# Optimization experiments

Measured on AMD Instinct MI355X. Metric: run time of the kernel, lower is better.

Reference implementation:

```python
import jax, jax.numpy as jnp
import numpy as np

CH = 512      # channels
CI = CH // 4  # in_channel = 128
DILS = (1, 4, 8, 12)
GN_GROUPS = 32


def conv2d(x, w, dil=1, pad=0):
    # x: (N,Cin,H,W), w: (Cout,Cin,kh,kw)
    return jax.lax.conv_general_dilated(
        x, w, window_strides=(1, 1), padding=[(pad, pad), (pad, pad)],
        rhs_dilation=(dil, dil),
        dimension_numbers=('NCHW', 'OIHW', 'NCHW'))


def group_norm(x, gamma, beta, groups=GN_GROUPS, eps=1e-5):
    N, C, H, W = x.shape
    xg = x.reshape(N, groups, C // groups, H, W)
    mu = jnp.mean(xg, axis=(2, 3, 4), keepdims=True)
    var = jnp.var(xg, axis=(2, 3, 4), keepdims=True)
    xn = ((xg - mu) * jax.lax.rsqrt(var + eps)).reshape(N, C, H, W)
    return xn * gamma[None, :, None, None] + beta[None, :, None, None]


def dyn_branch(xd, w_cat, d):
    # dynamic filter: (N, 9, H, W), softmax over the K=9 taps per pixel
    f = jax.nn.softmax(conv2d(xd, w_cat, dil=d, pad=d), axis=1)
    N, C, H, W = xd.shape
    xp = jnp.pad(xd, ((0, 0), (0, 0), (d, d), (d, d)))
    # fused unfold + weighted sum: accumulate 9 shifted views * per-pixel weight
    out = jnp.zeros_like(xd)
    k = 0
    for i in range(3):
        for j in range(3):
            out = out + xp[:, :, i * d:i * d + H, j * d:j * d + W] * f[:, k:k + 1]
            k += 1
    return out


def setup_inputs():
    key = jax.random.key(0)
    ks = jax.random.split(key, 16)
    s = 0.05
    return {
        'x': jax.random.normal(ks[0], (4, CH, 128, 128), jnp.float32),
        'w_scale1': jax.random.normal(ks[1], (CI, CH, 1, 1), jnp.float32) * s,
        'gn1_g': jnp.ones((CI,), jnp.float32),
        'gn1_b': jnp.zeros((CI,), jnp.float32),
        'w_cata': jax.random.normal(ks[2], (9, CI, 3, 3), jnp.float32) * s,
        'w_catb': jax.random.normal(ks[3], (9, CI, 3, 3), jnp.float32) * s,
        'w_catc': jax.random.normal(ks[4], (9, CI, 3, 3), jnp.float32) * s,
        'w_catd': jax.random.normal(ks[5], (9, CI, 3, 3), jnp.float32) * s,
        'w_scale2': jax.random.normal(ks[6], (CI, 5 * CI, 1, 1), jnp.float32) * s,
        'gn2_g': jnp.ones((CI,), jnp.float32),
        'gn2_b': jnp.zeros((CI,), jnp.float32),
        'w_scale3': jax.random.normal(ks[7], (CH, CI, 1, 1), jnp.float32) * s,
        'gn3_g': jnp.ones((CH,), jnp.float32),
        'gn3_b': jnp.zeros((CH,), jnp.float32),
    }


def reference(x, w_scale1, gn1_g, gn1_b, w_cata, w_catb, w_catc, w_catd,
              w_scale2, gn2_g, gn2_b, w_scale3, gn3_g, gn3_b):
    # scale1: 1x1 conv -> GN -> ReLU
    xd = jax.nn.relu(group_norm(conv2d(x, w_scale1), gn1_g, gn1_b))
    # four dilated dynamic-filter branches (unfold + softmax-weighted reduce)
    outs = [dyn_branch(xd, w, d)
            for w, d in zip((w_cata, w_catb, w_catc, w_catd), DILS)]
    cat = jnp.concatenate([xd] + outs, axis=1)  # (N, 5*CI, H, W)
    y = jax.nn.relu(group_norm(conv2d(cat, w_scale2), gn2_g, gn2_b))
    y = jax.nn.relu(group_norm(conv2d(y, w_scale3), gn3_g, gn3_b))
    return y
```

## Files before the change

kernel.cpp:

```cpp
#include <hip/hip_runtime.h>
#include <math.h>

#define HW 16384

typedef float f32x4 __attribute__((ext_vector_type(4)));
typedef __bf16 bf16x8 __attribute__((ext_vector_type(8)));
typedef unsigned short u16x4 __attribute__((ext_vector_type(4)));
typedef unsigned short u16x8 __attribute__((ext_vector_type(8)));

__device__ __forceinline__ unsigned short f2bf(float f) {
  unsigned u = __float_as_uint(f);
  u += 0x7fffu + ((u >> 16) & 1u);
  return (unsigned short)(u >> 16);
}
__device__ __forceinline__ float bf2f(unsigned short s) {
  return __uint_as_float(((unsigned)s) << 16);
}

__global__ void prep_kernel(const float* __restrict__ w1, const float* __restrict__ w2,
                            const float* __restrict__ w3,
                            const float* __restrict__ wa, const float* __restrict__ wb,
                            const float* __restrict__ wc, const float* __restrict__ wd,
                            unsigned short* __restrict__ w1b, unsigned short* __restrict__ w2b,
                            unsigned short* __restrict__ w3b, unsigned short* __restrict__ wr) {
  int idx = blockIdx.x * 256 + threadIdx.x;
  if (idx < 65536) { w1b[idx] = f2bf(w1[idx]); }
  else if (idx < 147456) { int j = idx - 65536; w2b[j] = f2bf(w2[j]); }
  else if (idx < 212992) { int j = idx - 147456; w3b[j] = f2bf(w3[j]); }
  else if (idx < 286720) {
    int j = idx - 212992;
    int br = j / 18432, rem = j % 18432;
    int tap = rem / 2048, rem2 = rem % 2048;
    int kt = rem2 / 128, c = rem2 % 128;
    const float* w = (br == 0) ? wa : (br == 1) ? wb : (br == 2) ? wc : wd;
    float v = (kt < 9) ? w[(kt * 128 + c) * 9 + tap] : 0.f;
    wr[j] = f2bf(v);
  }
}

__device__ __forceinline__ void gn_partial_epilogue(
    f32x4 (&acc)[8], int wv, int lane, int t, int n, int blkx,
    float* __restrict__ part, float (*ps)[32], float (*pss)[32]) {
  float gs[8], gss[8];
#pragma unroll
  for (int cb = 0; cb < 8; ++cb) {
    float s = 0.f, ss = 0.f;
#pragma unroll
    for (int r = 0; r < 4; ++r) { float v = acc[cb][r]; s += v; ss += v * v; }
#pragma unroll
    for (int m = 0; m < 4; ++m) {
      const int msk[4] = {1, 2, 16, 32};
      s += __shfl_xor(s, msk[m]); ss += __shfl_xor(ss, msk[m]);
    }
    gs[cb] = s; gss[cb] = ss;
  }
  if (lane < 16 && (lane & 3) == 0) {
    int q = lane >> 2;
#pragma unroll
    for (int cb = 0; cb < 8; ++cb) { ps[wv][cb * 4 + q] = gs[cb]; pss[wv][cb * 4 + q] = gss[cb]; }
  }
  __syncthreads();
  if (t < 32) {
    float a = ps[0][t] + ps[1][t] + ps[2][t] + ps[3][t];
    float b = pss[0][t] + pss[1][t] + pss[2][t] + pss[3][t];
    float* pp = part + ((size_t)(n * 32 + t) * 256 + blkx) * 2;
    pp[0] = a; pp[1] = b;
  }
}

__global__ __launch_bounds__(256) void conv1f_kernel(
    const float* __restrict__ x, const unsigned short* __restrict__ w1b,
    unsigned short* __restrict__ outb, float* __restrict__ part) {
  __shared__ float xs[2][64][68];
  __shared__ float ps[4][32], pss[4][32];
  int t = threadIdx.x;
  int wv = t >> 6, lane = t & 63, lr = lane & 15, lg = lane >> 4;
  int n = blockIdx.y;
  int p0 = blockIdx.x * 64;
  const float* xn = x + (size_t)n * 512 * HW + p0;
  f32x4 acc[8];
#pragma unroll
  for (int cb = 0; cb < 8; ++cb) acc[cb] = (f32x4){0.f, 0.f, 0.f, 0.f};

  int ci_l = t >> 4, px4 = (t & 15) * 4;
  float4 r[4];

#pragma unroll
  for (int pass = 0; pass < 4; ++pass)
    r[pass] = *(const float4*)(xn + (size_t)(pass * 16 + ci_l) * HW + px4);
#pragma unroll
  for (int pass = 0; pass < 4; ++pass) {
    int cl = pass * 16 + ci_l;
    xs[0][px4 + 0][cl] = r[pass].x; xs[0][px4 + 1][cl] = r[pass].y;
    xs[0][px4 + 2][cl] = r[pass].z; xs[0][px4 + 3][cl] = r[pass].w;
  }

  for (int kt = 0; kt < 8; ++kt) {
    int cur = kt & 1;
    if (kt < 7) {
#pragma unroll
      for (int pass = 0; pass < 4; ++pass)
        r[pass] = *(const float4*)(xn + (size_t)((kt + 1) * 64 + pass * 16 + ci_l) * HW + px4);
    }
    __syncthreads();
#pragma unroll
    for (int ks = 0; ks < 2; ++ks) {
      const float* arow = &xs[cur][wv * 16 + lr][ks * 32 + lg * 8];
      float4 a0 = *(const float4*)arow;
      float4 a1 = *(const float4*)(arow + 4);
      bf16x8 a;
      unsigned short us;
      us = f2bf(a0.x); a[0] = *(__bf16*)&us; us = f2bf(a0.y); a[1] = *(__bf16*)&us;
      us = f2bf(a0.z); a[2] = *(__bf16*)&us; us = f2bf(a0.w); a[3] = *(__bf16*)&us;
      us = f2bf(a1.x); a[4] = *(__bf16*)&us; us = f2bf(a1.y); a[5] = *(__bf16*)&us;
      us = f2bf(a1.z); a[6] = *(__bf16*)&us; us = f2bf(a1.w); a[7] = *(__bf16*)&us;
#pragma unroll
      for (int cb = 0; cb < 8; ++cb) {
        bf16x8 b = *(const bf16x8*)(w1b + (size_t)(cb * 16 + lr) * 512
                                    + kt * 64 + ks * 32 + lg * 8);
        acc[cb] = __builtin_amdgcn_mfma_f32_16x16x32_bf16(a, b, acc[cb], 0, 0, 0);
      }
    }
    if (kt < 7) {
#pragma unroll
      for (int pass = 0; pass < 4; ++pass) {
        int cl = pass * 16 + ci_l;
        xs[cur ^ 1][px4 + 0][cl] = r[pass].x; xs[cur ^ 1][px4 + 1][cl] = r[pass].y;
        xs[cur ^ 1][px4 + 2][cl] = r[pass].z; xs[cur ^ 1][px4 + 3][cl] = r[pass].w;
      }
    }
  }
  unsigned short* on = outb + (size_t)n * HW * 640;
#pragma unroll
  for (int cb = 0; cb < 8; ++cb)
#pragma unroll
    for (int r2 = 0; r2 < 4; ++r2)
      on[(size_t)(p0 + wv * 16 + lg * 4 + r2) * 640 + cb * 16 + lr] = f2bf(acc[cb][r2]);
  __syncthreads();
  gn_partial_epilogue(acc, wv, lane, t, n, blockIdx.x, part, ps, pss);
}

template<int K>
__global__ __launch_bounds__(256) void conv_pm_kernel(
    const unsigned short* __restrict__ act, const unsigned short* __restrict__ w,
    unsigned short* __restrict__ outb, float* __restrict__ part, int ldd) {
  __shared__ float ps[4][32], pss[4][32];
  int t = threadIdx.x;
  int wv = t >> 6, lane = t & 63;
  int lr = lane & 15, lg = lane >> 4;
  int n = blockIdx.y;
  int p0 = blockIdx.x * 64 + wv * 16;
  const unsigned short* an = act + (size_t)n * HW * K;
  f32x4 acc[8];
#pragma unroll
  for (int cb = 0; cb < 8; ++cb) acc[cb] = (f32x4){0.f, 0.f, 0.f, 0.f};
  const unsigned short* ap = an + (size_t)(p0 + lr) * K + lg * 8;
  const unsigned short* bp = w + (size_t)lr * K + lg * 8;
#pragma unroll 2
  for (int ks = 0; ks < K / 32; ++ks) {
    bf16x8 a = *(const bf16x8*)(ap + ks * 32);
#pragma unroll
    for (int cb = 0; cb < 8; ++cb) {
      bf16x8 b = *(const bf16x8*)(bp + (size_t)cb * 16 * K + ks * 32);
      acc[cb] = __builtin_amdgcn_mfma_f32_16x16x32_bf16(a, b, acc[cb], 0, 0, 0);
    }
  }
  unsigned short* on = outb + (size_t)n * HW * ldd;
#pragma unroll
  for (int cb = 0; cb < 8; ++cb)
#pragma unroll
    for (int r = 0; r < 4; ++r)
      on[(size_t)(p0 + lg * 4 + r) * ldd + cb * 16 + lr] = f2bf(acc[cb][r]);
  gn_partial_epilogue(acc, wv, lane, t, n, blockIdx.x, part, ps, pss);
}

__global__ __launch_bounds__(1024) void gnf256_kernel(
    const float* __restrict__ part, float* __restrict__ stats) {
  __shared__ float sh[1024], sh2[1024];
  int t = threadIdx.x;
  int tg = t >> 3, sub = t & 7;
  float s = 0.f, ss = 0.f;
  for (int b = sub * 32; b < sub * 32 + 32; ++b) {
    const float* pp = part + ((size_t)tg * 256 + b) * 2;
    s += pp[0]; ss += pp[1];
  }
  sh[t] = s; sh2[t] = ss;
  __syncthreads();
  if (t < 128) {
    float a = 0.f, b2 = 0.f;
#pragma unroll
    for (int i = 0; i < 8; ++i) { a += sh[t * 8 + i]; b2 += sh2[t * 8 + i]; }
    float inv = 1.f / (4.f * HW);
    float mean = a * inv, var = b2 * inv - mean * mean;
    stats[2 * t] = mean; stats[2 * t + 1] = rsqrtf(var + 1e-5f);
  }
}

__global__ __launch_bounds__(256) void gna_ip_kernel(
    unsigned short* __restrict__ dst, const float* __restrict__ stats,
    const float* __restrict__ gamma, const float* __restrict__ beta, int ldd) {
  int idx = blockIdx.x * 256 + threadIdx.x;
  int g = idx & 31;
  int p = (idx >> 5) & (HW - 1);
  int n = idx >> 19;
  unsigned short* ptr = dst + ((size_t)n * HW + p) * ldd + 4 * g;
  u16x4 v = *(u16x4*)ptr;
  int sg = n * 32 + g;
  float mean = stats[2 * sg], rstd = stats[2 * sg + 1];
  float sc0 = rstd * gamma[4 * g + 0], sc1 = rstd * gamma[4 * g + 1];
  float sc2 = rstd * gamma[4 * g + 2], sc3 = rstd * gamma[4 * g + 3];
  float sh0 = beta[4 * g + 0] - mean * sc0, sh1 = beta[4 * g + 1] - mean * sc1;
  float sh2 = beta[4 * g + 2] - mean * sc2, sh3 = beta[4 * g + 3] - mean * sc3;
  u16x4 o;
  o[0] = f2bf(fmaxf(fmaf(bf2f(v[0]), sc0, sh0), 0.f));
  o[1] = f2bf(fmaxf(fmaf(bf2f(v[1]), sc1, sh1), 0.f));
  o[2] = f2bf(fmaxf(fmaf(bf2f(v[2]), sc2, sh2), 0.f));
  o[3] = f2bf(fmaxf(fmaf(bf2f(v[3]), sc3, sh3), 0.f));
  *(u16x4*)ptr = o;
}

__global__ __launch_bounds__(256) void conv3_kernel(
    const unsigned short* __restrict__ y, const unsigned short* __restrict__ w3,
    unsigned short* __restrict__ outb, float* __restrict__ part) {
  int wv = threadIdx.x >> 6, lane = threadIdx.x & 63;
  int lr = lane & 15, lg = lane >> 4;
  int n = blockIdx.y, zc = blockIdx.z;
  int co0 = zc * 128 + wv * 32;
  int p0 = blockIdx.x * 128;
  const unsigned short* yn = y + (size_t)n * HW * 128;
  f32x4 acc[2][8];
#pragma unroll
  for (int pr = 0; pr < 2; ++pr)
#pragma unroll
    for (int cb = 0; cb < 8; ++cb) acc[pr][cb] = (f32x4){0.f, 0.f, 0.f, 0.f};
#pragma unroll
  for (int ks = 0; ks < 4; ++ks) {
    bf16x8 a0 = *(const bf16x8*)(w3 + (size_t)(co0 + lr) * 128 + ks * 32 + lg * 8);
    bf16x8 a1 = *(const bf16x8*)(w3 + (size_t)(co0 + 16 + lr) * 128 + ks * 32 + lg * 8);
#pragma unroll
    for (int cb = 0; cb < 8; ++cb) {
      bf16x8 b = *(const bf16x8*)(yn + (size_t)(p0 + cb * 16 + lr) * 128 + ks * 32 + lg * 8);
      acc[0][cb] = __builtin_amdgcn_mfma_f32_16x16x32_bf16(a0, b, acc[0][cb], 0, 0, 0);
      acc[1][cb] = __builtin_amdgcn_mfma_f32_16x16x32_bf16(a1, b, acc[1][cb], 0, 0, 0);
    }
  }
  unsigned short* on = outb + (size_t)n * 512 * HW;
  float s[2] = {0.f, 0.f}, ss[2] = {0.f, 0.f};
#pragma unroll
  for (int pr = 0; pr < 2; ++pr)
#pragma unroll
    for (int cb = 0; cb < 8; ++cb)
#pragma unroll
      for (int r = 0; r < 4; ++r) {
        float v = acc[pr][cb][r];
        on[(size_t)(co0 + pr * 16 + lg * 4 + r) * HW + p0 + cb * 16 + lr] = f2bf(v);
        s[pr] += v; ss[pr] += v * v;
      }
#pragma unroll
  for (int pr = 0; pr < 2; ++pr) {
    float a = s[pr], b = ss[pr];
    for (int m = 1; m < 64; m <<= 1) { a += __shfl_xor(a, m); b += __shfl_xor(b, m); }
    if (lane == 0) {
      float* pp = part + ((((size_t)n * 4 + zc) * 128 + blockIdx.x) * 8 + wv * 2 + pr) * 2;
      pp[0] = a; pp[1] = b;
    }
  }
}

__global__ __launch_bounds__(1024) void gnf3_kernel(
    const float* __restrict__ part, float* __restrict__ stats) {
  __shared__ float sh[1024], sh2[1024];
  int t = threadIdx.x;
  int e = t >> 3, xbs = t & 7;
  int n = e >> 5, g = e & 31;
  int zc = g >> 3, sub = g & 7;
  float s = 0.f, ss = 0.f;
  for (int xb = xbs * 16; xb < xbs * 16 + 16; ++xb) {
    const float* pp = part + ((((size_t)n * 4 + zc) * 128 + xb) * 8 + sub) * 2;
    s += pp[0]; ss += pp[1];
  }
  sh[t] = s; sh2[t] = ss;
  __syncthreads();
  if (t < 128) {
    float a = 0.f, b2 = 0.f;
#pragma unroll
    for (int i = 0; i < 8; ++i) { a += sh[t * 8 + i]; b2 += sh2[t * 8 + i]; }
    float inv = 1.f / (16.f * HW);
    float mean = a * inv, var = b2 * inv - mean * mean;
    stats[2 * t] = mean; stats[2 * t + 1] = rsqrtf(var + 1e-5f);
  }
}

__global__ __launch_bounds__(256) void gn3_apply_kernel(
    const unsigned short* __restrict__ y3b, const float* __restrict__ stats,
    const float* __restrict__ gamma, const float* __restrict__ beta,
    float* __restrict__ out) {
  size_t e8 = ((size_t)blockIdx.x * 256 + threadIdx.x) * 8;
  int n = (int)(e8 >> 23);
  int c = (int)((e8 >> 14) & 511);
  int sg = n * 32 + (c >> 4);
  float mean = stats[2 * sg], rstd = stats[2 * sg + 1];
  float scale = rstd * gamma[c];
  float shift = beta[c] - mean * scale;
  u16x8 u = *(const u16x8*)(y3b + e8);
  float4 o0, o1;
  o0.x = fmaxf(fmaf(bf2f(u[0]), scale, shift), 0.f);
  o0.y = fmaxf(fmaf(bf2f(u[1]), scale, shift), 0.f);
  o0.z = fmaxf(fmaf(bf2f(u[2]), scale, shift), 0.f);
  o0.w = fmaxf(fmaf(bf2f(u[3]), scale, shift), 0.f);
  o1.x = fmaxf(fmaf(bf2f(u[4]), scale, shift), 0.f);
  o1.y = fmaxf(fmaf(bf2f(u[5]), scale, shift), 0.f);
  o1.z = fmaxf(fmaf(bf2f(u[6]), scale, shift), 0.f);
  o1.w = fmaxf(fmaf(bf2f(u[7]), scale, shift), 0.f);
  *(float4*)(out + e8) = o0;
  *(float4*)(out + e8 + 4) = o1;
}

#define DP 136

__global__ __launch_bounds__(512, 4) void dynfused6_kernel(
    const unsigned short* __restrict__ cat, const unsigned short* __restrict__ wr,
    unsigned short* __restrict__ catw) {
  extern __shared__ char smem[];
  unsigned short* rowbuf = (unsigned short*)smem;
  float* fl = (float*)(smem + 3 * 88 * DP * 2);
  int t = threadIdx.x;
  int bid = blockIdx.x;
  int rh = ((bid & 7) << 5) + (bid >> 3);
  int row = rh >> 1, hw = rh & 1;
  int n = blockIdx.y >> 2, br = blockIdx.y & 3;
  int d = (br == 0) ? 1 : 4 * br;
  const unsigned short* xb = cat + (size_t)n * HW * 640;

  int rg[3] = { max(row - d, 0), row, min(row + d, 127) };
  bool rv[3] = { row - d >= 0, true, row + d < 128 };
  int cbase = hw * 64 - 12;

  {
    u16x8 vreg[9];
#pragma unroll
    for (int k = 0; k < 9; ++k) {
      int ci = t + (k << 9);
      if (k == 8 && ci >= 4224) continue;
      int s = (ci >= 2816) ? 2 : (ci >= 1408 ? 1 : 0);
      int rem = ci - s * 1408;
      int slot = rem >> 4, c = rem & 15;
      int gcol = min(max(cbase + slot, 0), 127);
      vreg[k] = *(const u16x8*)(xb + ((size_t)(rg[s] * 128 + gcol)) * 640 + c * 8);
    }
#pragma unroll
    for (int k = 0; k < 9; ++k) {
      int ci = t + (k << 9);
      if (k == 8 && ci >= 4224) continue;
      int s = (ci >= 2816) ? 2 : (ci >= 1408 ? 1 : 0);
      int rem = ci - s * 1408;
      int slot = rem >> 4, c = rem & 15;
      *(u16x8*)(rowbuf + ((size_t)s * 88 + slot) * DP + c * 8) = vreg[k];
    }
  }
  __syncthreads();

  if (t < 256) {
    int wv = t >> 6, lane = t & 63;
    int lr = lane & 15, lg = lane >> 4;
    const unsigned short* wb = wr + (size_t)br * 9 * 16 * 128;
    const bf16x8 zb = {(__bf16)0.f, (__bf16)0.f, (__bf16)0.f, (__bf16)0.f,
                       (__bf16)0.f, (__bf16)0.f, (__bf16)0.f, (__bf16)0.f};
    f32x4 acc = (f32x4){0.f, 0.f, 0.f, 0.f};
    int pxl = wv * 16 + lr;
    int gw = hw * 64 + pxl;
#pragma unroll
    for (int tap = 0; tap < 9; ++tap) {
      int s = tap / 3;
      int dw = (tap % 3 - 1) * d;
      int slot = 12 + pxl + dw;
      bool val = rv[s] && ((unsigned)(gw + dw) < 128u);
      const unsigned short* ap = rowbuf + ((size_t)s * 88 + slot) * DP + lg * 8;
      const unsigned short* wt = wb + (size_t)(tap * 16 + lr) * 128 + lg * 8;
#pragma unroll
      for (int ks = 0; ks < 4; ++ks) {
        bf16x8 a = *(const bf16x8*)(ap + ks * 32);
        if (!val) a = zb;
        bf16x8 b = *(const bf16x8*)(wt + ks * 32);
        acc = __builtin_amdgcn_mfma_f32_16x16x32_bf16(a, b, acc, 0, 0, 0);
      }
    }
#pragma unroll
    for (int r = 0; r < 4; ++r) {
      float v = acc[r];
      float m = (lr < 9) ? v : -3.0e38f;
#pragma unroll
      for (int msk = 1; msk < 16; msk <<= 1) m = fmaxf(m, __shfl_xor(m, msk));
      float e = (lr < 9) ? expf(v - m) : 0.f;
      float su = e;
#pragma unroll
      for (int msk = 1; msk < 16; msk <<= 1) su += __shfl_xor(su, msk);
      fl[(wv * 16 + lg * 4 + r) * 17 + lr] = e / su;
    }
  }
  __syncthreads();

  {
    int pxl = t >> 3, c8 = t & 7;
    int gw = hw * 64 + pxl;
    float oacc[16];
#pragma unroll
    for (int i = 0; i < 16; ++i) oacc[i] = 0.f;
#pragma unroll
    for (int tap = 0; tap < 9; ++tap) {
      int s = tap / 3;
      int dw = (tap % 3 - 1) * d;
      int slot = 12 + pxl + dw;
      bool val = rv[s] && ((unsigned)(gw + dw) < 128u);
      float f = val ? fl[pxl * 17 + tap] : 0.f;
      const unsigned short* ap = rowbuf + ((size_t)s * 88 + slot) * DP + c8 * 16;
#pragma unroll
      for (int cc = 0; cc < 2; ++cc) {
        u16x8 u = *(const u16x8*)(ap + cc * 8);
#pragma unroll
        for (int i = 0; i < 8; ++i)
          oacc[cc * 8 + i] = fmaf(f, bf2f(u[i]), oacc[cc * 8 + i]);
      }
    }
    unsigned short* orow = catw + ((size_t)n * HW + row * 128 + gw) * 640
                           + 128 * (br + 1) + c8 * 16;
#pragma unroll
    for (int cc = 0; cc < 2; ++cc) {
      u16x8 o;
#pragma unroll
      for (int i = 0; i < 8; ++i) o[i] = f2bf(oacc[cc * 8 + i]);
      *(u16x8*)(orow + cc * 8) = o;
    }
  }
}

extern "C" void kernel_launch(void* const* d_in, const int* in_sizes, int n_in,
                              void* d_out, int out_size, void* d_ws, size_t ws_size,
                              hipStream_t stream) {
  const float* x   = (const float*)d_in[0];
  const float* w1  = (const float*)d_in[1];
  const float* g1  = (const float*)d_in[2];
  const float* b1  = (const float*)d_in[3];
  const float* wca = (const float*)d_in[4];
  const float* wcb = (const float*)d_in[5];
  const float* wcc = (const float*)d_in[6];
  const float* wcd = (const float*)d_in[7];
  const float* w2  = (const float*)d_in[8];
  const float* g2  = (const float*)d_in[9];
  const float* b2  = (const float*)d_in[10];
  const float* w3  = (const float*)d_in[11];
  const float* g3  = (const float*)d_in[12];
  const float* b3  = (const float*)d_in[13];
  float* out = (float*)d_out;

  float* ws = (float*)d_ws;
  unsigned short* cat = (unsigned short*)(ws + 25165824);
  unsigned short* y2b = (unsigned short*)(ws + 8388608);
  unsigned short* y3b = (unsigned short*)(ws + 25165824);
  float* aux = ws + 46137344;
  unsigned short* w1b = (unsigned short*)(aux);
  unsigned short* w2b = (unsigned short*)(aux + 32768);
  unsigned short* w3b = (unsigned short*)(aux + 73728);
  unsigned short* wr  = (unsigned short*)(aux + 106496);
  float* part  = aux + 143360;
  float* part3 = aux + 208896;
  float* st1   = aux + 241664;
  float* st2   = aux + 241920;
  float* st3   = aux + 242176;

  dim3 blk(256);
  const int dynLds = 3 * 88 * DP * 2 + 64 * 17 * 4;
  (void)hipFuncSetAttribute((const void*)dynfused6_kernel,
                            hipFuncAttributeMaxDynamicSharedMemorySize, dynLds);

  prep_kernel<<<dim3(1120), blk, 0, stream>>>(w1, w2, w3, wca, wcb, wcc, wcd,
                                              w1b, w2b, w3b, wr);

  conv1f_kernel<<<dim3(256, 4), blk, 0, stream>>>(x, w1b, cat, part);
  gnf256_kernel<<<dim3(1), dim3(1024), 0, stream>>>(part, st1);
  gna_ip_kernel<<<dim3(8192), blk, 0, stream>>>(cat, st1, g1, b1, 640);

  dynfused6_kernel<<<dim3(256, 16), dim3(512), dynLds, stream>>>(cat, wr, cat);

  conv_pm_kernel<640><<<dim3(256, 4), blk, 0, stream>>>(cat, w2b, y2b, part, 128);
  gnf256_kernel<<<dim3(1), dim3(1024), 0, stream>>>(part, st2);
  gna_ip_kernel<<<dim3(8192), blk, 0, stream>>>(y2b, st2, g2, b2, 128);

  conv3_kernel<<<dim3(128, 4, 4), blk, 0, stream>>>(y2b, w3b, y3b, part3);
  gnf3_kernel<<<dim3(1), dim3(1024), 0, stream>>>(part3, st3);
  gn3_apply_kernel<<<dim3(16384), blk, 0, stream>>>(y3b, st3, g3, b3, out);
}
```

Before: 384.5 us.

## Recompute conv3 instead of storing it; transpose conv1 LDS tile layout

The final 1x1 conv is now run twice: a first pass computes only the GroupNorm statistics, and a second pass recomputes the matmul and applies GN+ReLU directly into the fp32 output. This removes the bf16 write and re-read of the 512-channel intermediate (about 64 MB of traffic) at the cost of doubling that conv's MFMA work and its y2 reads. The conv1 shared-memory tile is also transposed to a channel-major layout with odd padding, so stores are contiguous and reads become scalar strided accesses. The unroll pragma on the conv_pm K loop is removed as well.

```diff
diff --git a/kernel.cpp b/kernel.cpp
--- a/kernel.cpp
+++ b/kernel.cpp
@@ -71,7 +71,7 @@
 __global__ __launch_bounds__(256) void conv1f_kernel(
     const float* __restrict__ x, const unsigned short* __restrict__ w1b,
     unsigned short* __restrict__ outb, float* __restrict__ part) {
-  __shared__ float xs[2][64][68];
+  __shared__ float xs[2][64][65];
   __shared__ float ps[4][32], pss[4][32];
   int t = threadIdx.x;
   int wv = t >> 6, lane = t & 63, lr = lane & 15, lg = lane >> 4;
@@ -91,8 +91,8 @@
 #pragma unroll
   for (int pass = 0; pass < 4; ++pass) {
     int cl = pass * 16 + ci_l;
-    xs[0][px4 + 0][cl] = r[pass].x; xs[0][px4 + 1][cl] = r[pass].y;
-    xs[0][px4 + 2][cl] = r[pass].z; xs[0][px4 + 3][cl] = r[pass].w;
+    xs[0][cl][px4 + 0] = r[pass].x; xs[0][cl][px4 + 1] = r[pass].y;
+    xs[0][cl][px4 + 2] = r[pass].z; xs[0][cl][px4 + 3] = r[pass].w;
   }
 
   for (int kt = 0; kt < 8; ++kt) {
@@ -105,15 +105,12 @@
     __syncthreads();
 #pragma unroll
     for (int ks = 0; ks < 2; ++ks) {
-      const float* arow = &xs[cur][wv * 16 + lr][ks * 32 + lg * 8];
-      float4 a0 = *(const float4*)arow;
-      float4 a1 = *(const float4*)(arow + 4);
       bf16x8 a;
-      unsigned short us;
-      us = f2bf(a0.x); a[0] = *(__bf16*)&us; us = f2bf(a0.y); a[1] = *(__bf16*)&us;
-      us = f2bf(a0.z); a[2] = *(__bf16*)&us; us = f2bf(a0.w); a[3] = *(__bf16*)&us;
-      us = f2bf(a1.x); a[4] = *(__bf16*)&us; us = f2bf(a1.y); a[5] = *(__bf16*)&us;
-      us = f2bf(a1.z); a[6] = *(__bf16*)&us; us = f2bf(a1.w); a[7] = *(__bf16*)&us;
+#pragma unroll
+      for (int j = 0; j < 8; ++j) {
+        unsigned short us = f2bf(xs[cur][ks * 32 + lg * 8 + j][wv * 16 + lr]);
+        a[j] = *(__bf16*)&us;
+      }
 #pragma unroll
       for (int cb = 0; cb < 8; ++cb) {
         bf16x8 b = *(const bf16x8*)(w1b + (size_t)(cb * 16 + lr) * 512
@@ -125,8 +122,8 @@
 #pragma unroll
       for (int pass = 0; pass < 4; ++pass) {
         int cl = pass * 16 + ci_l;
-        xs[cur ^ 1][px4 + 0][cl] = r[pass].x; xs[cur ^ 1][px4 + 1][cl] = r[pass].y;
-        xs[cur ^ 1][px4 + 2][cl] = r[pass].z; xs[cur ^ 1][px4 + 3][cl] = r[pass].w;
+        xs[cur ^ 1][cl][px4 + 0] = r[pass].x; xs[cur ^ 1][cl][px4 + 1] = r[pass].y;
+        xs[cur ^ 1][cl][px4 + 2] = r[pass].z; xs[cur ^ 1][cl][px4 + 3] = r[pass].w;
       }
     }
   }
@@ -156,7 +153,6 @@
   for (int cb = 0; cb < 8; ++cb) acc[cb] = (f32x4){0.f, 0.f, 0.f, 0.f};
   const unsigned short* ap = an + (size_t)(p0 + lr) * K + lg * 8;
   const unsigned short* bp = w + (size_t)lr * K + lg * 8;
-#pragma unroll 2
   for (int ks = 0; ks < K / 32; ++ks) {
     bf16x8 a = *(const bf16x8*)(ap + ks * 32);
 #pragma unroll
@@ -219,9 +215,9 @@
   *(u16x4*)ptr = o;
 }
 
-__global__ __launch_bounds__(256) void conv3_kernel(
+__global__ __launch_bounds__(256) void conv3_stats_kernel(
     const unsigned short* __restrict__ y, const unsigned short* __restrict__ w3,
-    unsigned short* __restrict__ outb, float* __restrict__ part) {
+    float* __restrict__ part) {
   int wv = threadIdx.x >> 6, lane = threadIdx.x & 63;
   int lr = lane & 15, lg = lane >> 4;
   int n = blockIdx.y, zc = blockIdx.z;
@@ -244,7 +240,6 @@
       acc[1][cb] = __builtin_amdgcn_mfma_f32_16x16x32_bf16(a1, b, acc[1][cb], 0, 0, 0);
     }
   }
-  unsigned short* on = outb + (size_t)n * 512 * HW;
   float s[2] = {0.f, 0.f}, ss[2] = {0.f, 0.f};
 #pragma unroll
   for (int pr = 0; pr < 2; ++pr)
@@ -253,7 +248,6 @@
 #pragma unroll
       for (int r = 0; r < 4; ++r) {
         float v = acc[pr][cb][r];
-        on[(size_t)(co0 + pr * 16 + lg * 4 + r) * HW + p0 + cb * 16 + lr] = f2bf(v);
         s[pr] += v; ss[pr] += v * v;
       }
 #pragma unroll
@@ -291,29 +285,50 @@
   }
 }
 
-__global__ __launch_bounds__(256) void gn3_apply_kernel(
-    const unsigned short* __restrict__ y3b, const float* __restrict__ stats,
-    const float* __restrict__ gamma, const float* __restrict__ beta,
-    float* __restrict__ out) {
-  size_t e8 = ((size_t)blockIdx.x * 256 + threadIdx.x) * 8;
-  int n = (int)(e8 >> 23);
-  int c = (int)((e8 >> 14) & 511);
-  int sg = n * 32 + (c >> 4);
-  float mean = stats[2 * sg], rstd = stats[2 * sg + 1];
-  float scale = rstd * gamma[c];
-  float shift = beta[c] - mean * scale;
-  u16x8 u = *(const u16x8*)(y3b + e8);
-  float4 o0, o1;
-  o0.x = fmaxf(fmaf(bf2f(u[0]), scale, shift), 0.f);
-  o0.y = fmaxf(fmaf(bf2f(u[1]), scale, shift), 0.f);
-  o0.z = fmaxf(fmaf(bf2f(u[2]), scale, shift), 0.f);
-  o0.w = fmaxf(fmaf(bf2f(u[3]), scale, shift), 0.f);
-  o1.x = fmaxf(fmaf(bf2f(u[4]), scale, shift), 0.f);
-  o1.y = fmaxf(fmaf(bf2f(u[5]), scale, shift), 0.f);
-  o1.z = fmaxf(fmaf(bf2f(u[6]), scale, shift), 0.f);
-  o1.w = fmaxf(fmaf(bf2f(u[7]), scale, shift), 0.f);
-  *(float4*)(out + e8) = o0;
-  *(float4*)(out + e8 + 4) = o1;
+__global__ __launch_bounds__(256) void conv3_apply_kernel(
+    const unsigned short* __restrict__ y, const unsigned short* __restrict__ w3,
+    const float* __restrict__ stats, const float* __restrict__ gamma,
+    const float* __restrict__ beta, float* __restrict__ out) {
+  int wv = threadIdx.x >> 6, lane = threadIdx.x & 63;
+  int lr = lane & 15, lg = lane >> 4;
+  int n = blockIdx.y, zc = blockIdx.z;
+  int co0 = zc * 128 + wv * 32;
+  int p0 = blockIdx.x * 128;
+  const unsigned short* yn = y + (size_t)n * HW * 128;
+  f32x4 acc[2][8];
+#pragma unroll
+  for (int pr = 0; pr < 2; ++pr)
+#pragma unroll
+    for (int cb = 0; cb < 8; ++cb) acc[pr][cb] = (f32x4){0.f, 0.f, 0.f, 0.f};
+#pragma unroll
+  for (int ks = 0; ks < 4; ++ks) {
+    bf16x8 a0 = *(const bf16x8*)(w3 + (size_t)(co0 + lr) * 128 + ks * 32 + lg * 8);
+    bf16x8 a1 = *(const bf16x8*)(w3 + (size_t)(co0 + 16 + lr) * 128 + ks * 32 + lg * 8);
+#pragma unroll
+    for (int cb = 0; cb < 8; ++cb) {
+      bf16x8 b = *(const bf16x8*)(yn + (size_t)(p0 + cb * 16 + lr) * 128 + ks * 32 + lg * 8);
+      acc[0][cb] = __builtin_amdgcn_mfma_f32_16x16x32_bf16(a0, b, acc[0][cb], 0, 0, 0);
+      acc[1][cb] = __builtin_amdgcn_mfma_f32_16x16x32_bf16(a1, b, acc[1][cb], 0, 0, 0);
+    }
+  }
+  float* on = out + (size_t)n * 512 * HW;
+#pragma unroll
+  for (int pr = 0; pr < 2; ++pr) {
+    int gbase = zc * 8 + wv * 2 + pr;
+    int sg = n * 32 + gbase;
+    float mean = stats[2 * sg], rstd = stats[2 * sg + 1];
+#pragma unroll
+    for (int r = 0; r < 4; ++r) {
+      int co = co0 + pr * 16 + lg * 4 + r;
+      float sc = rstd * gamma[co];
+      float sh = beta[co] - mean * sc;
+#pragma unroll
+      for (int cb = 0; cb < 8; ++cb) {
+        float v = fmaxf(fmaf(acc[pr][cb][r], sc, sh), 0.f);
+        on[(size_t)co * HW + p0 + cb * 16 + lr] = v;
+      }
+    }
+  }
 }
 
 #define DP 136
@@ -456,7 +471,6 @@
   float* ws = (float*)d_ws;
   unsigned short* cat = (unsigned short*)(ws + 25165824);
   unsigned short* y2b = (unsigned short*)(ws + 8388608);
-  unsigned short* y3b = (unsigned short*)(ws + 25165824);
   float* aux = ws + 46137344;
   unsigned short* w1b = (unsigned short*)(aux);
   unsigned short* w2b = (unsigned short*)(aux + 32768);
@@ -486,7 +500,7 @@
   gnf256_kernel<<<dim3(1), dim3(1024), 0, stream>>>(part, st2);
   gna_ip_kernel<<<dim3(8192), blk, 0, stream>>>(y2b, st2, g2, b2, 128);
 
-  conv3_kernel<<<dim3(128, 4, 4), blk, 0, stream>>>(y2b, w3b, y3b, part3);
+  conv3_stats_kernel<<<dim3(128, 4, 4), blk, 0, stream>>>(y2b, w3b, part3);
   gnf3_kernel<<<dim3(1), dim3(1024), 0, stream>>>(part3, st3);
-  gn3_apply_kernel<<<dim3(16384), blk, 0, stream>>>(y3b, st3, g3, b3, out);
-}
+  conv3_apply_kernel<<<dim3(128, 4, 4), blk, 0, stream>>>(y2b, w3b, st3, g3, b3, out);
+}
```

Measured after the change: 390.3 us. No clear change (+1.5%).
